# Optimization experiments

Hardware: AMD Instinct MI355X
Metric: run time of the kernel (lower is better)

## Reference

```python
import jax, jax.numpy as jnp
import numpy as np

EMB = 768
B, LD, LW, LH = 2, 8, 8, 8        # LR grid = number of windows per axis
HD, HW, HH = 32, 32, 32           # HR volume
LN_EPS = 1e-5


def setup_inputs() -> dict:
    key = jax.random.key(0)
    ks = jax.random.split(key, 12)
    s = 1.0 / np.sqrt(EMB)
    inp = {
        "LR_image": jax.random.normal(ks[0], (B, LD, LW, LH, EMB), jnp.float32),
        "HR_image": jax.random.normal(ks[1], (B, HD, HW, HH, EMB), jnp.float32),
        "Wq_w": jax.random.uniform(ks[2], (EMB, EMB), jnp.float32, -s, s),
        "Wq_b": jax.random.uniform(ks[3], (EMB,), jnp.float32, -s, s),
        "Wk_w": jax.random.uniform(ks[4], (EMB, EMB), jnp.float32, -s, s),
        "Wk_b": jax.random.uniform(ks[5], (EMB,), jnp.float32, -s, s),
        "Wv_w": jax.random.uniform(ks[6], (EMB, EMB), jnp.float32, -s, s),
        "Wv_b": jax.random.uniform(ks[7], (EMB,), jnp.float32, -s, s),
        "Wo_w": jax.random.uniform(ks[8], (EMB, EMB), jnp.float32, -s, s),
        "Wo_b": jax.random.uniform(ks[9], (EMB,), jnp.float32, -s, s),
        "ln_g": jnp.ones((EMB,), jnp.float32),
        "ln_b": jnp.zeros((EMB,), jnp.float32),
        "S_d": 4, "S_w": 4, "S_h": 4,
    }
    return inp


def _window_partition(x, S_d, S_w, S_h):
    # x: [B, D, W, H, C] -> [B, N_blocks, S_d*S_w*S_h, C]
    b, d, w, h, c = x.shape
    x = x.reshape(b, d // S_d, S_d, w // S_w, S_w, h // S_h, S_h, c)
    x = jnp.transpose(x, (0, 2, 4, 6, 1, 3, 5, 7))  # [B,Sd,Sw,Sh,Db,Wb,Hb,C]
    x = x.reshape(b, S_d * S_w * S_h, -1, c)
    return jnp.transpose(x, (0, 2, 1, 3))  # [B, N_blocks, S, C]


def reference(LR_image, HR_image, Wq_w, Wq_b, Wk_w, Wk_b, Wv_w, Wv_b,
              Wo_w, Wo_b, ln_g, ln_b, S_d, S_w, S_h):
    b = LR_image.shape[0]
    c = LR_image.shape[-1]
    # queries: [B, N, 1, C]
    q_in = LR_image.reshape(b, -1, c)[:, :, None, :]
    # windowed keys/values: [B, N, S, C]
    hr = _window_partition(HR_image, S_d, S_w, S_h)
    q = q_in @ Wq_w.T + Wq_b
    k = hr @ Wk_w.T + Wk_b
    v = hr @ Wv_w.T + Wv_b
    scale = 1.0 / jnp.sqrt(jnp.asarray(c, q.dtype))
    scores = jnp.einsum('bnqc,bnsc->bnqs', q, k) * scale  # [B,N,1,S]
    attn = jax.nn.softmax(scores, axis=-1)
    x = jnp.einsum('bnqs,bnsc->bnqc', attn, v).reshape(b, -1, c)
    x = x @ Wo_w.T + Wo_b
    res = q.reshape(b, -1, c) + x  # residual with projected queries
    mu = jnp.mean(res, axis=-1, keepdims=True)
    var = jnp.var(res, axis=-1, keepdims=True)
    return (res - mu) / jnp.sqrt(var + LN_EPS) * ln_g + ln_b
```

## Files before the change

### kernel.cpp

```cpp
#include <hip/hip_runtime.h>
#include <hip/hip_bf16.h>
#include <math.h>

#define EMB 768
#define NB 2
#define NWIN 512
#define NROWS (NB*NWIN)
#define SWIN 64
#define HRDIM 32
#define ROWF (NROWS*EMB)
#define WELEM (EMB*EMB)

using bfrag = __attribute__((ext_vector_type(8))) short;
using f32x4 = __attribute__((ext_vector_type(4))) float;

#define GL16(g, l)  __builtin_amdgcn_global_load_lds(                         \
    (const __attribute__((address_space(1))) void*)(g),                       \
    (__attribute__((address_space(3))) void*)(l), 16, 0, 0)

__global__ __launch_bounds__(256)
void prep_kernel(const float* __restrict__ LR, __hip_bfloat16* __restrict__ LRb,
                 const float* __restrict__ Wq, __hip_bfloat16* __restrict__ Wqb,
                 const float* __restrict__ Wo, __hip_bfloat16* __restrict__ Wob,
                 const float* __restrict__ Wk, __hip_bfloat16* __restrict__ WkTb,
                 const float* __restrict__ Wv, __hip_bfloat16* __restrict__ WvTb,
                 const float* __restrict__ bv, const float* __restrict__ bo,
                 float* __restrict__ bvo) {
  __shared__ float tile[32][33];
  const int bx = blockIdx.x;
  const int t = threadIdx.x;

  if (bx < 960) {
    const float* in; __hip_bfloat16* out; int i;
    if (bx < 384)      { in = LR; out = LRb; i = bx * 256 + t; }
    else if (bx < 672) { in = Wq; out = Wqb; i = (bx - 384) * 256 + t; }
    else               { in = Wo; out = Wob; i = (bx - 672) * 256 + t; }
    float4 a = *(const float4*)&in[(size_t)i * 8];
    float4 b = *(const float4*)&in[(size_t)i * 8 + 4];
    __hip_bfloat16 o[8];
    o[0] = __float2bfloat16(a.x); o[1] = __float2bfloat16(a.y);
    o[2] = __float2bfloat16(a.z); o[3] = __float2bfloat16(a.w);
    o[4] = __float2bfloat16(b.x); o[5] = __float2bfloat16(b.y);
    o[6] = __float2bfloat16(b.z); o[7] = __float2bfloat16(b.w);
    *(uint4*)&out[(size_t)i * 8] = *(const uint4*)o;
  } else if (bx < 2112) {
    int idx = bx - 960;
    int z = idx / 576, rem = idx % 576;
    int bi = rem % 24, bj = rem / 24;
    const float* in; __hip_bfloat16* out;
    if (z == 0) { in = Wk; out = WkTb; }
    else        { in = Wv; out = WvTb; }
    const int c = t & 31, r8 = t >> 5;
#pragma unroll
    for (int rr = 0; rr < 4; ++rr) {
      int r = r8 + rr * 8;
      tile[c][r] = in[(size_t)(bi * 32 + r) * EMB + bj * 32 + c];
    }
    __syncthreads();
#pragma unroll
    for (int rr = 0; rr < 4; ++rr) {
      int n = r8 + rr * 8;
      out[(size_t)(bj * 32 + n) * EMB + bi * 32 + c] = __float2bfloat16(tile[n][c]);
    }
  } else {
    int idx = bx - 2112;
    const int w = t >> 6, lane = t & 63;
    const int p = idx * 4 + w;
    float s = 0.f;
#pragma unroll
    for (int r = 0; r < 12; ++r) {
      int n = lane + r * 64;
      s = fmaf(Wo[(size_t)p * EMB + n], bv[n], s);
    }
#pragma unroll
    for (int o = 32; o > 0; o >>= 1) s += __shfl_xor(s, o, 64);
    if (lane == 0) bvo[p] = bo[p] + s;
  }
}

__global__ __launch_bounds__(256)
void gemm64(const __hip_bfloat16* __restrict__ A0,
            const __hip_bfloat16* __restrict__ B0,
            const float* __restrict__ bias0, float* __restrict__ Cf0,
            __hip_bfloat16* __restrict__ Cb0, const float* __restrict__ R0,
            const __hip_bfloat16* __restrict__ A1,
            const __hip_bfloat16* __restrict__ B1,
            const float* __restrict__ bias1, float* __restrict__ Cf1,
            __hip_bfloat16* __restrict__ Cb1,
            int N, int ylim1) {
  constexpr int K = EMB;
  constexpr int NT = K / 64;
  const int zi = blockIdx.z;
  const __hip_bfloat16* A  = zi ? A1 : A0;
  const __hip_bfloat16* Bm = zi ? B1 : B0;
  const float* bias = zi ? bias1 : bias0;
  float* Cf = zi ? Cf1 : Cf0;
  __hip_bfloat16* Cb = zi ? Cb1 : Cb0;
  const float* R = zi ? nullptr : R0;

  if (zi == 1 && (int)blockIdx.y >= ylim1) return;

  __shared__ short lsA[3][64 * 64];
  __shared__ short lsB[3][64 * 64];
  const int t = threadIdx.x;
  const int w = t >> 6, lane = t & 63;
  const int lr = lane & 15, lk = lane >> 4;
  const int m0 = blockIdx.y * 64, n0 = blockIdx.x * 64;

  const int r0 = t >> 3, c0 = t & 7;
  const int kc = c0 ^ (r0 & 7);
  const __hip_bfloat16* aptr0 = A + (size_t)(m0 + r0) * K + kc * 8;
  const __hip_bfloat16* aptr1 = A + (size_t)(m0 + r0 + 32) * K + kc * 8;
  const __hip_bfloat16* bptr0 = Bm + (size_t)(n0 + r0) * K + kc * 8;
  const __hip_bfloat16* bptr1 = Bm + (size_t)(n0 + r0 + 32) * K + kc * 8;
  const int wbase = w * 512;

  const int arow = w * 16 + lr;
  int aoff[2], boff[4][2];
#pragma unroll
  for (int ks = 0; ks < 2; ++ks)
    aoff[ks] = arow * 64 + (((ks << 2) | lk) ^ (arow & 7)) * 8;
#pragma unroll
  for (int f = 0; f < 4; ++f) {
    int br = f * 16 + lr;
#pragma unroll
    for (int ks = 0; ks < 2; ++ks)
      boff[f][ks] = br * 64 + (((ks << 2) | lk) ^ (br & 7)) * 8;
  }

  f32x4 acc[4];
#pragma unroll
  for (int f = 0; f < 4; ++f) acc[f] = (f32x4){0.f, 0.f, 0.f, 0.f};

#pragma unroll
  for (int p = 0; p < 2; ++p) {
    int ko = p * 64;
    GL16(aptr0 + ko, &lsA[p][wbase]);
    GL16(aptr1 + ko, &lsA[p][wbase + 2048]);
    GL16(bptr0 + ko, &lsB[p][wbase]);
    GL16(bptr1 + ko, &lsB[p][wbase + 2048]);
  }

#pragma unroll
  for (int kt = 0; kt < NT; ++kt) {
    if (kt + 2 < NT) {
      constexpr int s3[NT + 2] = {0,1,2,0,1,2,0,1,2,0,1,2,0,1};
      const int sl = s3[kt + 2];
      int ko = (kt + 2) * 64;
      GL16(aptr0 + ko, &lsA[sl][wbase]);
      GL16(aptr1 + ko, &lsA[sl][wbase + 2048]);
      GL16(bptr0 + ko, &lsB[sl][wbase]);
      GL16(bptr1 + ko, &lsB[sl][wbase + 2048]);
    }
    if (kt + 2 < NT)      asm volatile("s_waitcnt vmcnt(8)" ::: "memory");
    else if (kt + 1 < NT) asm volatile("s_waitcnt vmcnt(4)" ::: "memory");
    else                  asm volatile("s_waitcnt vmcnt(0)" ::: "memory");
    __builtin_amdgcn_sched_barrier(0);
    __builtin_amdgcn_s_barrier();

    const int cur = kt % 3;
    bfrag a0 = *(const bfrag*)&lsA[cur][aoff[0]];
    bfrag a1 = *(const bfrag*)&lsA[cur][aoff[1]];
    bfrag b00 = *(const bfrag*)&lsB[cur][boff[0][0]];
    bfrag b01 = *(const bfrag*)&lsB[cur][boff[0][1]];
    bfrag b10 = *(const bfrag*)&lsB[cur][boff[1][0]];
    bfrag b11 = *(const bfrag*)&lsB[cur][boff[1][1]];
    bfrag b20 = *(const bfrag*)&lsB[cur][boff[2][0]];
    bfrag b21 = *(const bfrag*)&lsB[cur][boff[2][1]];
    bfrag b30 = *(const bfrag*)&lsB[cur][boff[3][0]];
    bfrag b31 = *(const bfrag*)&lsB[cur][boff[3][1]];
    acc[0] = __builtin_amdgcn_mfma_f32_16x16x32_bf16(a0, b00, acc[0], 0, 0, 0);
    acc[0] = __builtin_amdgcn_mfma_f32_16x16x32_bf16(a1, b01, acc[0], 0, 0, 0);
    acc[1] = __builtin_amdgcn_mfma_f32_16x16x32_bf16(a0, b10, acc[1], 0, 0, 0);
    acc[1] = __builtin_amdgcn_mfma_f32_16x16x32_bf16(a1, b11, acc[1], 0, 0, 0);
    acc[2] = __builtin_amdgcn_mfma_f32_16x16x32_bf16(a0, b20, acc[2], 0, 0, 0);
    acc[2] = __builtin_amdgcn_mfma_f32_16x16x32_bf16(a1, b21, acc[2], 0, 0, 0);
    acc[3] = __builtin_amdgcn_mfma_f32_16x16x32_bf16(a0, b30, acc[3], 0, 0, 0);
    acc[3] = __builtin_amdgcn_mfma_f32_16x16x32_bf16(a1, b31, acc[3], 0, 0, 0);

    asm volatile("s_waitcnt lgkmcnt(0)" ::: "memory");
    __builtin_amdgcn_s_barrier();
    __builtin_amdgcn_sched_barrier(0);
  }

  float bs[4];
#pragma unroll
  for (int f = 0; f < 4; ++f)
    bs[f] = bias ? bias[n0 + f * 16 + lr] : 0.f;

#pragma unroll
  for (int f = 0; f < 4; ++f) {
    int n = n0 + f * 16 + lr;
#pragma unroll
    for (int j = 0; j < 4; ++j) {
      int m = m0 + w * 16 + lk * 4 + j;
      float v = acc[f][j] + bs[f];
      if (R)  v += R[(size_t)m * N + n];
      if (Cf) Cf[(size_t)m * N + n] = v;
      if (Cb) Cb[(size_t)m * N + n] = __float2bfloat16(v);
    }
  }
}

__global__ __launch_bounds__(512)
void attn_kernel(const float* __restrict__ HR, const float* __restrict__ qt,
                 __hip_bfloat16* __restrict__ zb) {
  const int g = blockIdx.x;
  const int b = g >> 9;
  const int n = g & 511;
  const int db = n >> 6, wb = (n >> 3) & 7, hb = n & 7;

  __shared__ float zp[8][EMB];
  __shared__ float ml[8][2];

  const int t = threadIdx.x;
  const int w = t >> 6, lane = t & 63;

  float4 qv[3];
#pragma unroll
  for (int r = 0; r < 3; ++r)
    qv[r] = *(const float4*)&qt[(size_t)g * EMB + (lane + r * 64) * 4];

  const float* rows[8];
#pragma unroll
  for (int i = 0; i < 8; ++i) {
    int s = w * 8 + i;
    int D = db * 4 + (s >> 4), W = wb * 4 + ((s >> 2) & 3), H = hb * 4 + (s & 3);
    rows[i] = HR + (size_t)((((b * HRDIM + D) * HRDIM + W) * HRDIM + H)) * EMB;
  }

  const float scale = 0.036084391824351615f;
  float m = -3.0e38f, l = 0.f;
  float4 z0 = {0,0,0,0}, z1 = {0,0,0,0}, z2 = {0,0,0,0};

  float4 h0 = *(const float4*)&rows[0][lane * 4];
  float4 h1 = *(const float4*)&rows[0][(lane + 64) * 4];
  float4 h2 = *(const float4*)&rows[0][(lane + 128) * 4];

#pragma unroll
  for (int i = 0; i < 8; ++i) {
    float4 n0, n1, n2;
    if (i < 7) {
      n0 = *(const float4*)&rows[i + 1][lane * 4];
      n1 = *(const float4*)&rows[i + 1][(lane + 64) * 4];
      n2 = *(const float4*)&rows[i + 1][(lane + 128) * 4];
    }
    float p = 0.f;
    p = fmaf(h0.x, qv[0].x, p); p = fmaf(h0.y, qv[0].y, p);
    p = fmaf(h0.z, qv[0].z, p); p = fmaf(h0.w, qv[0].w, p);
    p = fmaf(h1.x, qv[1].x, p); p = fmaf(h1.y, qv[1].y, p);
    p = fmaf(h1.z, qv[1].z, p); p = fmaf(h1.w, qv[1].w, p);
    p = fmaf(h2.x, qv[2].x, p); p = fmaf(h2.y, qv[2].y, p);
    p = fmaf(h2.z, qv[2].z, p); p = fmaf(h2.w, qv[2].w, p);
#pragma unroll
    for (int o = 32; o > 0; o >>= 1) p += __shfl_xor(p, o, 64);
    p *= scale;
    float mn = fmaxf(m, p);
    float f = expf(m - mn);
    float e = expf(p - mn);
    z0.x = fmaf(e, h0.x, z0.x * f); z0.y = fmaf(e, h0.y, z0.y * f);
    z0.z = fmaf(e, h0.z, z0.z * f); z0.w = fmaf(e, h0.w, z0.w * f);
    z1.x = fmaf(e, h1.x, z1.x * f); z1.y = fmaf(e, h1.y, z1.y * f);
    z1.z = fmaf(e, h1.z, z1.z * f); z1.w = fmaf(e, h1.w, z1.w * f);
    z2.x = fmaf(e, h2.x, z2.x * f); z2.y = fmaf(e, h2.y, z2.y * f);
    z2.z = fmaf(e, h2.z, z2.z * f); z2.w = fmaf(e, h2.w, z2.w * f);
    l = fmaf(l, f, e);
    m = mn;
    if (i < 7) { h0 = n0; h1 = n1; h2 = n2; }
  }

  *(float4*)&zp[w][lane * 4] = z0;
  *(float4*)&zp[w][(lane + 64) * 4] = z1;
  *(float4*)&zp[w][(lane + 128) * 4] = z2;
  if (lane == 0) { ml[w][0] = m; ml[w][1] = l; }
  __syncthreads();

  if (t < 384) {
    float M = -3.0e38f;
#pragma unroll
    for (int w8 = 0; w8 < 8; ++w8) M = fmaxf(M, ml[w8][0]);
    float L = 0.f, a0 = 0.f, a1 = 0.f;
#pragma unroll
    for (int w8 = 0; w8 < 8; ++w8) {
      float ew = expf(ml[w8][0] - M);
      L = fmaf(ml[w8][1], ew, L);
      float2 v = *(const float2*)&zp[w8][t * 2];
      a0 = fmaf(v.x, ew, a0);
      a1 = fmaf(v.y, ew, a1);
    }
    float rl = 1.f / L;
    __hip_bfloat16 o[2];
    o[0] = __float2bfloat16(a0 * rl);
    o[1] = __float2bfloat16(a1 * rl);
    *(unsigned*)&zb[(size_t)g * EMB + t * 2] = *(const unsigned*)o;
  }
}

__global__ __launch_bounds__(256)
void ln_kernel(const float* __restrict__ R, const float* __restrict__ gma,
               const float* __restrict__ bta, float* __restrict__ out) {
  const int row = blockIdx.x;
  const int t = threadIdx.x;
  const int wave = t >> 6, lane = t & 63;
  __shared__ float red[4];

  float v[3];
  float s = 0.f;
#pragma unroll
  for (int r = 0; r < 3; ++r) {
    int c = t + r * 256;
    v[r] = R[(size_t)row * EMB + c];
    s += v[r];
  }
#pragma unroll
  for (int o = 32; o > 0; o >>= 1) s += __shfl_xor(s, o, 64);
  if (lane == 0) red[wave] = s;
  __syncthreads();
  float mu = (red[0] + red[1] + red[2] + red[3]) * (1.f / EMB);
  __syncthreads();

  float q = 0.f;
#pragma unroll
  for (int r = 0; r < 3; ++r) {
    float d = v[r] - mu;
    q += d * d;
  }
#pragma unroll
  for (int o = 32; o > 0; o >>= 1) q += __shfl_xor(q, o, 64);
  if (lane == 0) red[wave] = q;
  __syncthreads();
  float var = (red[0] + red[1] + red[2] + red[3]) * (1.f / EMB);
  float inv = rsqrtf(var + 1e-5f);

#pragma unroll
  for (int r = 0; r < 3; ++r) {
    int c = t + r * 256;
    out[(size_t)row * EMB + c] = (v[r] - mu) * inv * gma[c] + bta[c];
  }
}

extern "C" void kernel_launch(void* const* d_in, const int* in_sizes, int n_in,
                              void* d_out, int out_size, void* d_ws, size_t ws_size,
                              hipStream_t stream) {
  const float* LR  = (const float*)d_in[0];
  const float* HR  = (const float*)d_in[1];
  const float* Wq  = (const float*)d_in[2];
  const float* bq  = (const float*)d_in[3];
  const float* Wk  = (const float*)d_in[4];
  const float* Wv  = (const float*)d_in[6];
  const float* bv  = (const float*)d_in[7];
  const float* Wo  = (const float*)d_in[8];
  const float* bo  = (const float*)d_in[9];
  const float* lng = (const float*)d_in[10];
  const float* lnb = (const float*)d_in[11];
  float* out = (float*)d_out;

  char* ws = (char*)d_ws;
  float* Qf = (float*)(ws + 0);
  float* qt = (float*)(ws + 3145728);
  float* x  = (float*)(ws + 6291456);
  __hip_bfloat16* LRb  = (__hip_bfloat16*)(ws +  9437184);
  __hip_bfloat16* zb   = (__hip_bfloat16*)(ws + 11010048);
  __hip_bfloat16* Qbb  = (__hip_bfloat16*)(ws + 12582912);
  __hip_bfloat16* Wqb  = (__hip_bfloat16*)(ws + 14155776);
  __hip_bfloat16* WkTb = (__hip_bfloat16*)(ws + 15335424);
  __hip_bfloat16* WvTb = (__hip_bfloat16*)(ws + 16515072);
  __hip_bfloat16* Wob  = (__hip_bfloat16*)(ws + 17694720);
  __hip_bfloat16* Wvob = (__hip_bfloat16*)(ws + 18874368);
  float* bvo = (float*)(ws + 20054016);

  dim3 blk(256);

  prep_kernel<<<dim3(2304), blk, 0, stream>>>(
      LR, LRb, Wq, Wqb, Wo, Wob, Wk, WkTb, Wv, WvTb, bv, bo, bvo);

  gemm64<<<dim3(12, 16, 2), blk, 0, stream>>>(
      LRb, Wqb, bq, Qf, Qbb, nullptr,
      Wob, WvTb, nullptr, nullptr, Wvob,
      EMB, 12);

  gemm64<<<dim3(12, 16, 1), blk, 0, stream>>>(
      Qbb, WkTb, nullptr, qt, nullptr, nullptr,
      nullptr, nullptr, nullptr, nullptr, nullptr,
      EMB, 0);

  attn_kernel<<<dim3(NROWS), dim3(512), 0, stream>>>(HR, qt, zb);

  gemm64<<<dim3(12, 16, 1), blk, 0, stream>>>(
      zb, Wvob, bvo, x, nullptr, Qf,
      nullptr, nullptr, nullptr, nullptr, nullptr,
      EMB, 0);

  ln_kernel<<<dim3(NROWS), blk, 0, stream>>>(x, lng, lnb, out);
}
```

Baseline: 76.05 us.

## Split-K the query-key projection GEMM and use nontemporal HR loads in attention

Replaces the single qt GEMM (192 blocks) with a split-K variant that launches two K-halves over 384 blocks, each writing a partial fp32 result. The attention kernel then sums the two partials when it loads the query vector. HR loads become nontemporal, and the online-softmax updates are written with vector arithmetic. The goal is better CU occupancy for the small GEMM and less cache pollution from streaming HR, at the cost of an extra 3 MB partial buffer to write and read.

```diff
diff --git a/kernel.cpp b/kernel.cpp
--- a/kernel.cpp
+++ b/kernel.cpp
@@ -202,8 +202,113 @@
   }
 }
 
+__global__ __launch_bounds__(256)
+void gemm64_k2(const __hip_bfloat16* __restrict__ A,
+               const __hip_bfloat16* __restrict__ Bm,
+               float* __restrict__ Cf, int N) {
+  constexpr int K = EMB;
+  constexpr int NT = 6;
+  const int zi = blockIdx.z;
+  const int koff = zi * 384;
+  float* Cout = Cf + (size_t)zi * ROWF;
+
+  __shared__ short lsA[3][64 * 64];
+  __shared__ short lsB[3][64 * 64];
+  const int t = threadIdx.x;
+  const int w = t >> 6, lane = t & 63;
+  const int lr = lane & 15, lk = lane >> 4;
+  const int m0 = blockIdx.y * 64, n0 = blockIdx.x * 64;
+
+  const int r0 = t >> 3, c0 = t & 7;
+  const int kc = c0 ^ (r0 & 7);
+  const __hip_bfloat16* aptr0 = A + (size_t)(m0 + r0) * K + koff + kc * 8;
+  const __hip_bfloat16* aptr1 = A + (size_t)(m0 + r0 + 32) * K + koff + kc * 8;
+  const __hip_bfloat16* bptr0 = Bm + (size_t)(n0 + r0) * K + koff + kc * 8;
+  const __hip_bfloat16* bptr1 = Bm + (size_t)(n0 + r0 + 32) * K + koff + kc * 8;
+  const int wbase = w * 512;
+
+  const int arow = w * 16 + lr;
+  int aoff[2], boff[4][2];
+#pragma unroll
+  for (int ks = 0; ks < 2; ++ks)
+    aoff[ks] = arow * 64 + (((ks << 2) | lk) ^ (arow & 7)) * 8;
+#pragma unroll
+  for (int f = 0; f < 4; ++f) {
+    int br = f * 16 + lr;
+#pragma unroll
+    for (int ks = 0; ks < 2; ++ks)
+      boff[f][ks] = br * 64 + (((ks << 2) | lk) ^ (br & 7)) * 8;
+  }
+
+  f32x4 acc[4];
+#pragma unroll
+  for (int f = 0; f < 4; ++f) acc[f] = (f32x4){0.f, 0.f, 0.f, 0.f};
+
+#pragma unroll
+  for (int p = 0; p < 2; ++p) {
+    int ko = p * 64;
+    GL16(aptr0 + ko, &lsA[p][wbase]);
+    GL16(aptr1 + ko, &lsA[p][wbase + 2048]);
+    GL16(bptr0 + ko, &lsB[p][wbase]);
+    GL16(bptr1 + ko, &lsB[p][wbase + 2048]);
+  }
+
+#pragma unroll
+  for (int kt = 0; kt < NT; ++kt) {
+    if (kt + 2 < NT) {
+      constexpr int s3[NT + 2] = {0,1,2,0,1,2,0,1};
+      const int sl = s3[kt + 2];
+      int ko = (kt + 2) * 64;
+      GL16(aptr0 + ko, &lsA[sl][wbase]);
+      GL16(aptr1 + ko, &lsA[sl][wbase + 2048]);
+      GL16(bptr0 + ko, &lsB[sl][wbase]);
+      GL16(bptr1 + ko, &lsB[sl][wbase + 2048]);
+    }
+    if (kt + 2 < NT)      asm volatile("s_waitcnt vmcnt(8)" ::: "memory");
+    else if (kt + 1 < NT) asm volatile("s_waitcnt vmcnt(4)" ::: "memory");
+    else                  asm volatile("s_waitcnt vmcnt(0)" ::: "memory");
+    __builtin_amdgcn_sched_barrier(0);
+    __builtin_amdgcn_s_barrier();
+
+    const int cur = kt % 3;
+    bfrag a0 = *(const bfrag*)&lsA[cur][aoff[0]];
+    bfrag a1 = *(const bfrag*)&lsA[cur][aoff[1]];
+    bfrag b00 = *(const bfrag*)&lsB[cur][boff[0][0]];
+    bfrag b01 = *(const bfrag*)&lsB[cur][boff[0][1]];
+    bfrag b10 = *(const bfrag*)&lsB[cur][boff[1][0]];
+    bfrag b11 = *(const bfrag*)&lsB[cur][boff[1][1]];
+    bfrag b20 = *(const bfrag*)&lsB[cur][boff[2][0]];
+    bfrag b21 = *(const bfrag*)&lsB[cur][boff[2][1]];
+    bfrag b30 = *(const bfrag*)&lsB[cur][boff[3][0]];
+    bfrag b31 = *(const bfrag*)&lsB[cur][boff[3][1]];
+    acc[0] = __builtin_amdgcn_mfma_f32_16x16x32_bf16(a0, b00, acc[0], 0, 0, 0);
+    acc[0] = __builtin_amdgcn_mfma_f32_16x16x32_bf16(a1, b01, acc[0], 0, 0, 0);
+    acc[1] = __builtin_amdgcn_mfma_f32_16x16x32_bf16(a0, b10, acc[1], 0, 0, 0);
+    acc[1] = __builtin_amdgcn_mfma_f32_16x16x32_bf16(a1, b11, acc[1], 0, 0, 0);
+    acc[2] = __builtin_amdgcn_mfma_f32_16x16x32_bf16(a0, b20, acc[2], 0, 0, 0);
+    acc[2] = __builtin_amdgcn_mfma_f32_16x16x32_bf16(a1, b21, acc[2], 0, 0, 0);
+    acc[3] = __builtin_amdgcn_mfma_f32_16x16x32_bf16(a0, b30, acc[3], 0, 0, 0);
+    acc[3] = __builtin_amdgcn_mfma_f32_16x16x32_bf16(a1, b31, acc[3], 0, 0, 0);
+
+    asm volatile("s_waitcnt lgkmcnt(0)" ::: "memory");
+    __builtin_amdgcn_s_barrier();
+    __builtin_amdgcn_sched_barrier(0);
+  }
+
+#pragma unroll
+  for (int f = 0; f < 4; ++f) {
+    int n = n0 + f * 16 + lr;
+#pragma unroll
+    for (int j = 0; j < 4; ++j) {
+      int m = m0 + w * 16 + lk * 4 + j;
+      Cout[(size_t)m * N + n] = acc[f][j];
+    }
+  }
+}
+
 __global__ __launch_bounds__(512)
-void attn_kernel(const float* __restrict__ HR, const float* __restrict__ qt,
+void attn_kernel(const float* __restrict__ HR, const float* __restrict__ qtp0,
+                 const float* __restrict__ qtp1,
                  __hip_bfloat16* __restrict__ zb) {
   const int g = blockIdx.x;
   const int b = g >> 9;
@@ -216,10 +321,13 @@
   const int t = threadIdx.x;
   const int w = t >> 6, lane = t & 63;
 
-  float4 qv[3];
-#pragma unroll
-  for (int r = 0; r < 3; ++r)
-    qv[r] = *(const float4*)&qt[(size_t)g * EMB + (lane + r * 64) * 4];
+  f32x4 qv[3];
+#pragma unroll
+  for (int r = 0; r < 3; ++r) {
+    f32x4 a = *(const f32x4*)&qtp0[(size_t)g * EMB + (lane + r * 64) * 4];
+    f32x4 c = *(const f32x4*)&qtp1[(size_t)g * EMB + (lane + r * 64) * 4];
+    qv[r] = a + c;
+  }
 
   const float* rows[8];
 #pragma unroll
@@ -231,47 +339,44 @@
 
   const float scale = 0.036084391824351615f;
   float m = -3.0e38f, l = 0.f;
-  float4 z0 = {0,0,0,0}, z1 = {0,0,0,0}, z2 = {0,0,0,0};
-
-  float4 h0 = *(const float4*)&rows[0][lane * 4];
-  float4 h1 = *(const float4*)&rows[0][(lane + 64) * 4];
-  float4 h2 = *(const float4*)&rows[0][(lane + 128) * 4];
+  f32x4 z0 = {0,0,0,0}, z1 = {0,0,0,0}, z2 = {0,0,0,0};
+
+  f32x4 h0 = __builtin_nontemporal_load((const f32x4*)&rows[0][lane * 4]);
+  f32x4 h1 = __builtin_nontemporal_load((const f32x4*)&rows[0][(lane + 64) * 4]);
+  f32x4 h2 = __builtin_nontemporal_load((const f32x4*)&rows[0][(lane + 128) * 4]);
 
 #pragma unroll
   for (int i = 0; i < 8; ++i) {
-    float4 n0, n1, n2;
+    f32x4 n0, n1, n2;
     if (i < 7) {
-      n0 = *(const float4*)&rows[i + 1][lane * 4];
-      n1 = *(const float4*)&rows[i + 1][(lane + 64) * 4];
-      n2 = *(const float4*)&rows[i + 1][(lane + 128) * 4];
+      n0 = __builtin_nontemporal_load((const f32x4*)&rows[i + 1][lane * 4]);
+      n1 = __builtin_nontemporal_load((const f32x4*)&rows[i + 1][(lane + 64) * 4]);
+      n2 = __builtin_nontemporal_load((const f32x4*)&rows[i + 1][(lane + 128) * 4]);
     }
     float p = 0.f;
-    p = fmaf(h0.x, qv[0].x, p); p = fmaf(h0.y, qv[0].y, p);
-    p = fmaf(h0.z, qv[0].z, p); p = fmaf(h0.w, qv[0].w, p);
-    p = fmaf(h1.x, qv[1].x, p); p = fmaf(h1.y, qv[1].y, p);
-    p = fmaf(h1.z, qv[1].z, p); p = fmaf(h1.w, qv[1].w, p);
-    p = fmaf(h2.x, qv[2].x, p); p = fmaf(h2.y, qv[2].y, p);
-    p = fmaf(h2.z, qv[2].z, p); p = fmaf(h2.w, qv[2].w, p);
+#pragma unroll
+    for (int c = 0; c < 4; ++c) p = fmaf(h0[c], qv[0][c], p);
+#pragma unroll
+    for (int c = 0; c < 4; ++c) p = fmaf(h1[c], qv[1][c], p);
+#pragma unroll
+    for (int c = 0; c < 4; ++c) p = fmaf(h2[c], qv[2][c], p);
 #pragma unroll
     for (int o = 32; o > 0; o >>= 1) p += __shfl_xor(p, o, 64);
     p *= scale;
     float mn = fmaxf(m, p);
     float f = expf(m - mn);
     float e = expf(p - mn);
-    z0.x = fmaf(e, h0.x, z0.x * f); z0.y = fmaf(e, h0.y, z0.y * f);
-    z0.z = fmaf(e, h0.z, z0.z * f); z0.w = fmaf(e, h0.w, z0.w * f);
-    z1.x = fmaf(e, h1.x, z1.x * f); z1.y = fmaf(e, h1.y, z1.y * f);
-    z1.z = fmaf(e, h1.z, z1.z * f); z1.w = fmaf(e, h1.w, z1.w * f);
-    z2.x = fmaf(e, h2.x, z2.x * f); z2.y = fmaf(e, h2.y, z2.y * f);
-    z2.z = fmaf(e, h2.z, z2.z * f); z2.w = fmaf(e, h2.w, z2.w * f);
+    z0 = z0 * f + h0 * e;
+    z1 = z1 * f + h1 * e;
+    z2 = z2 * f + h2 * e;
     l = fmaf(l, f, e);
     m = mn;
     if (i < 7) { h0 = n0; h1 = n1; h2 = n2; }
   }
 
-  *(float4*)&zp[w][lane * 4] = z0;
-  *(float4*)&zp[w][(lane + 64) * 4] = z1;
-  *(float4*)&zp[w][(lane + 128) * 4] = z2;
+  *(f32x4*)&zp[w][lane * 4] = z0;
+  *(f32x4*)&zp[w][(lane + 64) * 4] = z1;
+  *(f32x4*)&zp[w][(lane + 128) * 4] = z2;
   if (lane == 0) { ml[w][0] = m; ml[w][1] = l; }
   __syncthreads();
 
@@ -356,18 +461,18 @@
   float* out = (float*)d_out;
 
   char* ws = (char*)d_ws;
-  float* Qf = (float*)(ws + 0);
-  float* qt = (float*)(ws + 3145728);
-  float* x  = (float*)(ws + 6291456);
-  __hip_bfloat16* LRb  = (__hip_bfloat16*)(ws +  9437184);
-  __hip_bfloat16* zb   = (__hip_bfloat16*)(ws + 11010048);
-  __hip_bfloat16* Qbb  = (__hip_bfloat16*)(ws + 12582912);
-  __hip_bfloat16* Wqb  = (__hip_bfloat16*)(ws + 14155776);
-  __hip_bfloat16* WkTb = (__hip_bfloat16*)(ws + 15335424);
-  __hip_bfloat16* WvTb = (__hip_bfloat16*)(ws + 16515072);
-  __hip_bfloat16* Wob  = (__hip_bfloat16*)(ws + 17694720);
-  __hip_bfloat16* Wvob = (__hip_bfloat16*)(ws + 18874368);
-  float* bvo = (float*)(ws + 20054016);
+  float* Qf  = (float*)(ws + 0);
+  float* qtp = (float*)(ws + 3145728);
+  float* x   = (float*)(ws + 9437184);
+  __hip_bfloat16* LRb  = (__hip_bfloat16*)(ws + 12582912);
+  __hip_bfloat16* zb   = (__hip_bfloat16*)(ws + 14155776);
+  __hip_bfloat16* Qbb  = (__hip_bfloat16*)(ws + 15728640);
+  __hip_bfloat16* Wqb  = (__hip_bfloat16*)(ws + 17301504);
+  __hip_bfloat16* WkTb = (__hip_bfloat16*)(ws + 18481152);
+  __hip_bfloat16* WvTb = (__hip_bfloat16*)(ws + 19660800);
+  __hip_bfloat16* Wob  = (__hip_bfloat16*)(ws + 20840448);
+  __hip_bfloat16* Wvob = (__hip_bfloat16*)(ws + 22020096);
+  float* bvo = (float*)(ws + 23199744);
 
   dim3 blk(256);
 
@@ -379,12 +484,10 @@
       Wob, WvTb, nullptr, nullptr, Wvob,
       EMB, 12);
 
-  gemm64<<<dim3(12, 16, 1), blk, 0, stream>>>(
-      Qbb, WkTb, nullptr, qt, nullptr, nullptr,
-      nullptr, nullptr, nullptr, nullptr, nullptr,
-      EMB, 0);
-
-  attn_kernel<<<dim3(NROWS), dim3(512), 0, stream>>>(HR, qt, zb);
+  gemm64_k2<<<dim3(12, 16, 2), blk, 0, stream>>>(Qbb, WkTb, qtp, EMB);
+
+  attn_kernel<<<dim3(NROWS), dim3(512), 0, stream>>>(
+      HR, qtp, qtp + (size_t)ROWF, zb);
 
   gemm64<<<dim3(12, 16, 1), blk, 0, stream>>>(
       zb, Wvob, bvo, x, nullptr, Qf,
```

After: 76.54 us. About the same (+0.6%).

## Fuse fp32-to-bf16 conversion into Q projection GEMM and merge launches

Applied to the files above, without the earlier changes.

The separate prep kernel that converted LR and Wq to bf16 is removed. The Q projection GEMM now loads fp32 operands directly, converts them in registers and stores them swizzled into LDS, while a second z-slice of the same launch transposes and converts the Wk, Wv and Wo weights and computes the fused bias. The q·Wk GEMM is then batched with the Wo·Wv GEMM into one launch. This removes a kernel launch and the bf16 staging round-trip through memory. In exchange the GEMM reads fp32 operands, doubling its load traffic, and the prep work is serialized onto 192 blocks.

```diff
diff --git a/kernel.cpp b/kernel.cpp
--- a/kernel.cpp
+++ b/kernel.cpp
@@ -18,63 +18,173 @@
     (const __attribute__((address_space(1))) void*)(g),                       \
     (__attribute__((address_space(3))) void*)(l), 16, 0, 0)
 
+__device__ __forceinline__ uint4 cvt8(float4 a, float4 b) {
+  __hip_bfloat16 o[8];
+  o[0] = __float2bfloat16(a.x); o[1] = __float2bfloat16(a.y);
+  o[2] = __float2bfloat16(a.z); o[3] = __float2bfloat16(a.w);
+  o[4] = __float2bfloat16(b.x); o[5] = __float2bfloat16(b.y);
+  o[6] = __float2bfloat16(b.z); o[7] = __float2bfloat16(b.w);
+  return *(const uint4*)o;
+}
+
 __global__ __launch_bounds__(256)
-void prep_kernel(const float* __restrict__ LR, __hip_bfloat16* __restrict__ LRb,
-                 const float* __restrict__ Wq, __hip_bfloat16* __restrict__ Wqb,
-                 const float* __restrict__ Wo, __hip_bfloat16* __restrict__ Wob,
-                 const float* __restrict__ Wk, __hip_bfloat16* __restrict__ WkTb,
-                 const float* __restrict__ Wv, __hip_bfloat16* __restrict__ WvTb,
-                 const float* __restrict__ bv, const float* __restrict__ bo,
-                 float* __restrict__ bvo) {
+void gemmA_kernel(const float* __restrict__ LR, const float* __restrict__ Wq,
+                  const float* __restrict__ bq, float* __restrict__ Qf,
+                  __hip_bfloat16* __restrict__ Qbb,
+                  const float* __restrict__ Wk, __hip_bfloat16* __restrict__ WkTb,
+                  const float* __restrict__ Wv, __hip_bfloat16* __restrict__ WvTb,
+                  const float* __restrict__ Wo, __hip_bfloat16* __restrict__ Wob,
+                  const float* __restrict__ bv, const float* __restrict__ bo,
+                  float* __restrict__ bvo) {
+  __shared__ short lsA[2][64 * 64];
+  __shared__ short lsB[2][64 * 64];
   __shared__ float tile[32][33];
-  const int bx = blockIdx.x;
   const int t = threadIdx.x;
 
-  if (bx < 960) {
-    const float* in; __hip_bfloat16* out; int i;
-    if (bx < 384)      { in = LR; out = LRb; i = bx * 256 + t; }
-    else if (bx < 672) { in = Wq; out = Wqb; i = (bx - 384) * 256 + t; }
-    else               { in = Wo; out = Wob; i = (bx - 672) * 256 + t; }
-    float4 a = *(const float4*)&in[(size_t)i * 8];
-    float4 b = *(const float4*)&in[(size_t)i * 8 + 4];
-    __hip_bfloat16 o[8];
-    o[0] = __float2bfloat16(a.x); o[1] = __float2bfloat16(a.y);
-    o[2] = __float2bfloat16(a.z); o[3] = __float2bfloat16(a.w);
-    o[4] = __float2bfloat16(b.x); o[5] = __float2bfloat16(b.y);
-    o[6] = __float2bfloat16(b.z); o[7] = __float2bfloat16(b.w);
-    *(uint4*)&out[(size_t)i * 8] = *(const uint4*)o;
-  } else if (bx < 2112) {
-    int idx = bx - 960;
-    int z = idx / 576, rem = idx % 576;
-    int bi = rem % 24, bj = rem / 24;
-    const float* in; __hip_bfloat16* out;
-    if (z == 0) { in = Wk; out = WkTb; }
-    else        { in = Wv; out = WvTb; }
-    const int c = t & 31, r8 = t >> 5;
-#pragma unroll
-    for (int rr = 0; rr < 4; ++rr) {
-      int r = r8 + rr * 8;
-      tile[c][r] = in[(size_t)(bi * 32 + r) * EMB + bj * 32 + c];
-    }
-    __syncthreads();
-#pragma unroll
-    for (int rr = 0; rr < 4; ++rr) {
-      int n = r8 + rr * 8;
-      out[(size_t)(bj * 32 + n) * EMB + bi * 32 + c] = __float2bfloat16(tile[n][c]);
-    }
-  } else {
-    int idx = bx - 2112;
-    const int w = t >> 6, lane = t & 63;
-    const int p = idx * 4 + w;
-    float s = 0.f;
-#pragma unroll
-    for (int r = 0; r < 12; ++r) {
-      int n = lane + r * 64;
-      s = fmaf(Wo[(size_t)p * EMB + n], bv[n], s);
-    }
-#pragma unroll
-    for (int o = 32; o > 0; o >>= 1) s += __shfl_xor(s, o, 64);
-    if (lane == 0) bvo[p] = bo[p] + s;
+  if (blockIdx.z == 1) {
+    const int bf = blockIdx.y * 12 + blockIdx.x;
+    for (int it = 0; it < 9; ++it) {
+      int j = bf + it * 192;
+      if (j < 1152) {
+        const float* in = (j < 576) ? Wk : Wv;
+        __hip_bfloat16* out = (j < 576) ? WkTb : WvTb;
+        int jj = (j < 576) ? j : j - 576;
+        int bi = jj % 24, bj = jj / 24;
+        const int c = t & 31, r8 = t >> 5;
+#pragma unroll
+        for (int rr = 0; rr < 4; ++rr) {
+          int r = r8 + rr * 8;
+          tile[c][r] = in[(size_t)(bi * 32 + r) * EMB + bj * 32 + c];
+        }
+        __syncthreads();
+#pragma unroll
+        for (int rr = 0; rr < 4; ++rr) {
+          int n = r8 + rr * 8;
+          out[(size_t)(bj * 32 + n) * EMB + bi * 32 + c] =
+              __float2bfloat16(tile[n][c]);
+        }
+        __syncthreads();
+      } else if (j < 1440) {
+        int i = (j - 1152) * 256 + t;
+        float4 a = *(const float4*)&Wo[(size_t)i * 8];
+        float4 b = *(const float4*)&Wo[(size_t)i * 8 + 4];
+        *(uint4*)&Wob[(size_t)i * 8] = cvt8(a, b);
+      } else if (j < 1632) {
+        const int w = t >> 6, lane = t & 63;
+        const int p = (j - 1440) * 4 + w;
+        float s = 0.f;
+#pragma unroll
+        for (int r = 0; r < 12; ++r) {
+          int n = lane + r * 64;
+          s = fmaf(Wo[(size_t)p * EMB + n], bv[n], s);
+        }
+#pragma unroll
+        for (int o = 32; o > 0; o >>= 1) s += __shfl_xor(s, o, 64);
+        if (lane == 0) bvo[p] = bo[p] + s;
+      }
+    }
+    return;
+  }
+
+  const int w = t >> 6, lane = t & 63;
+  const int lr = lane & 15, lk = lane >> 4;
+  const int m0 = blockIdx.y * 64, n0 = blockIdx.x * 64;
+  const int r0 = t >> 3, c0 = t & 7;
+
+  const float* ga0 = LR + (size_t)(m0 + r0) * EMB + c0 * 8;
+  const float* ga1 = LR + (size_t)(m0 + r0 + 32) * EMB + c0 * 8;
+  const float* gb0 = Wq + (size_t)(n0 + r0) * EMB + c0 * 8;
+  const float* gb1 = Wq + (size_t)(n0 + r0 + 32) * EMB + c0 * 8;
+  const int sl8 = (c0 ^ (r0 & 7)) * 8;
+  const int wA0 = r0 * 64 + sl8, wA1 = (r0 + 32) * 64 + sl8;
+
+  const int arow = w * 16 + lr;
+  int aoff[2], boff[4][2];
+#pragma unroll
+  for (int ks = 0; ks < 2; ++ks)
+    aoff[ks] = arow * 64 + (((ks << 2) | lk) ^ (arow & 7)) * 8;
+#pragma unroll
+  for (int f = 0; f < 4; ++f) {
+    int br = f * 16 + lr;
+#pragma unroll
+    for (int ks = 0; ks < 2; ++ks)
+      boff[f][ks] = br * 64 + (((ks << 2) | lk) ^ (br & 7)) * 8;
+  }
+
+  float4 bufA[2][4], bufB[2][4];
+#define LOADT(ph, ko)                                                         \
+  do {                                                                        \
+    bufA[ph][0] = *(const float4*)(ga0 + (ko));                               \
+    bufA[ph][1] = *(const float4*)(ga0 + (ko) + 4);                           \
+    bufA[ph][2] = *(const float4*)(ga1 + (ko));                               \
+    bufA[ph][3] = *(const float4*)(ga1 + (ko) + 4);                           \
+    bufB[ph][0] = *(const float4*)(gb0 + (ko));                               \
+    bufB[ph][1] = *(const float4*)(gb0 + (ko) + 4);                           \
+    bufB[ph][2] = *(const float4*)(gb1 + (ko));                               \
+    bufB[ph][3] = *(const float4*)(gb1 + (ko) + 4);                           \
+  } while (0)
+#define STORET(ph, sl)                                                        \
+  do {                                                                        \
+    *(uint4*)&lsA[sl][wA0] = cvt8(bufA[ph][0], bufA[ph][1]);                  \
+    *(uint4*)&lsA[sl][wA1] = cvt8(bufA[ph][2], bufA[ph][3]);                  \
+    *(uint4*)&lsB[sl][wA0] = cvt8(bufB[ph][0], bufB[ph][1]);                  \
+    *(uint4*)&lsB[sl][wA1] = cvt8(bufB[ph][2], bufB[ph][3]);                  \
+  } while (0)
+
+  f32x4 acc[4];
+#pragma unroll
+  for (int f = 0; f < 4; ++f) acc[f] = (f32x4){0.f, 0.f, 0.f, 0.f};
+
+  LOADT(0, 0);
+  LOADT(1, 64);
+  STORET(0, 0);
+  asm volatile("s_waitcnt lgkmcnt(0)" ::: "memory");
+  __builtin_amdgcn_s_barrier();
+
+#pragma unroll
+  for (int kt = 0; kt < 12; ++kt) {
+    const int cur = kt & 1, nxt = cur ^ 1;
+    if (kt + 2 < 12) LOADT(cur, (kt + 2) * 64);
+    if (kt + 1 < 12) STORET(nxt, nxt);
+    bfrag a0 = *(const bfrag*)&lsA[cur][aoff[0]];
+    bfrag a1 = *(const bfrag*)&lsA[cur][aoff[1]];
+    bfrag b00 = *(const bfrag*)&lsB[cur][boff[0][0]];
+    bfrag b01 = *(const bfrag*)&lsB[cur][boff[0][1]];
+    bfrag b10 = *(const bfrag*)&lsB[cur][boff[1][0]];
+    bfrag b11 = *(const bfrag*)&lsB[cur][boff[1][1]];
+    bfrag b20 = *(const bfrag*)&lsB[cur][boff[2][0]];
+    bfrag b21 = *(const bfrag*)&lsB[cur][boff[2][1]];
+    bfrag b30 = *(const bfrag*)&lsB[cur][boff[3][0]];
+    bfrag b31 = *(const bfrag*)&lsB[cur][boff[3][1]];
+    acc[0] = __builtin_amdgcn_mfma_f32_16x16x32_bf16(a0, b00, acc[0], 0, 0, 0);
+    acc[0] = __builtin_amdgcn_mfma_f32_16x16x32_bf16(a1, b01, acc[0], 0, 0, 0);
+    acc[1] = __builtin_amdgcn_mfma_f32_16x16x32_bf16(a0, b10, acc[1], 0, 0, 0);
+    acc[1] = __builtin_amdgcn_mfma_f32_16x16x32_bf16(a1, b11, acc[1], 0, 0, 0);
+    acc[2] = __builtin_amdgcn_mfma_f32_16x16x32_bf16(a0, b20, acc[2], 0, 0, 0);
+    acc[2] = __builtin_amdgcn_mfma_f32_16x16x32_bf16(a1, b21, acc[2], 0, 0, 0);
+    acc[3] = __builtin_amdgcn_mfma_f32_16x16x32_bf16(a0, b30, acc[3], 0, 0, 0);
+    acc[3] = __builtin_amdgcn_mfma_f32_16x16x32_bf16(a1, b31, acc[3], 0, 0, 0);
+
+    asm volatile("s_waitcnt lgkmcnt(0)" ::: "memory");
+    __builtin_amdgcn_s_barrier();
+    __builtin_amdgcn_sched_barrier(0);
+  }
+#undef LOADT
+#undef STORET
+
+  float bs[4];
+#pragma unroll
+  for (int f = 0; f < 4; ++f) bs[f] = bq[n0 + f * 16 + lr];
+#pragma unroll
+  for (int f = 0; f < 4; ++f) {
+    int n = n0 + f * 16 + lr;
+#pragma unroll
+    for (int j = 0; j < 4; ++j) {
+      int m = m0 + w * 16 + lk * 4 + j;
+      float v = acc[f][j] + bs[f];
+      Qf[(size_t)m * EMB + n] = v;
+      Qbb[(size_t)m * EMB + n] = __float2bfloat16(v);
+    }
   }
 }
 
@@ -359,30 +469,23 @@
   float* Qf = (float*)(ws + 0);
   float* qt = (float*)(ws + 3145728);
   float* x  = (float*)(ws + 6291456);
-  __hip_bfloat16* LRb  = (__hip_bfloat16*)(ws +  9437184);
-  __hip_bfloat16* zb   = (__hip_bfloat16*)(ws + 11010048);
-  __hip_bfloat16* Qbb  = (__hip_bfloat16*)(ws + 12582912);
-  __hip_bfloat16* Wqb  = (__hip_bfloat16*)(ws + 14155776);
-  __hip_bfloat16* WkTb = (__hip_bfloat16*)(ws + 15335424);
-  __hip_bfloat16* WvTb = (__hip_bfloat16*)(ws + 16515072);
-  __hip_bfloat16* Wob  = (__hip_bfloat16*)(ws + 17694720);
-  __hip_bfloat16* Wvob = (__hip_bfloat16*)(ws + 18874368);
-  float* bvo = (float*)(ws + 20054016);
+  __hip_bfloat16* zb   = (__hip_bfloat16*)(ws +  9437184);
+  __hip_bfloat16* Qbb  = (__hip_bfloat16*)(ws + 11010048);
+  __hip_bfloat16* WkTb = (__hip_bfloat16*)(ws + 12582912);
+  __hip_bfloat16* WvTb = (__hip_bfloat16*)(ws + 13762560);
+  __hip_bfloat16* Wvob = (__hip_bfloat16*)(ws + 14942208);
+  __hip_bfloat16* Wob  = (__hip_bfloat16*)(ws + 16121856);
+  float* bvo = (float*)(ws + 17301504);
 
   dim3 blk(256);
 
-  prep_kernel<<<dim3(2304), blk, 0, stream>>>(
-      LR, LRb, Wq, Wqb, Wo, Wob, Wk, WkTb, Wv, WvTb, bv, bo, bvo);
+  gemmA_kernel<<<dim3(12, 16, 2), blk, 0, stream>>>(
+      LR, Wq, bq, Qf, Qbb, Wk, WkTb, Wv, WvTb, Wo, Wob, bv, bo, bvo);
 
   gemm64<<<dim3(12, 16, 2), blk, 0, stream>>>(
-      LRb, Wqb, bq, Qf, Qbb, nullptr,
+      Qbb, WkTb, nullptr, qt, nullptr, nullptr,
       Wob, WvTb, nullptr, nullptr, Wvob,
       EMB, 12);
-
-  gemm64<<<dim3(12, 16, 1), blk, 0, stream>>>(
-      Qbb, WkTb, nullptr, qt, nullptr, nullptr,
-      nullptr, nullptr, nullptr, nullptr, nullptr,
-      EMB, 0);
 
   attn_kernel<<<dim3(NROWS), dim3(512), 0, stream>>>(HR, qt, zb);
 
```

After: 77.63 us. +2.1%, slower.
